# Performance work log

Measured on AMD Instinct MI355X. Metric: run time of the kernel, lower is better.

Reference implementation:

```python
import jax, jax.numpy as jnp
import numpy as np

LN_EPS = 1e-5


def setup_inputs() -> dict:
    key = jax.random.key(0)
    ks = jax.random.split(key, 6)
    N, E, D = 100000, 600000, 128
    x = jax.random.normal(ks[0], (N, D), dtype=jnp.float32)
    edge_index = jax.random.randint(ks[1], (2, E), 0, N, dtype=jnp.int64)
    dropout_mask = jax.random.uniform(ks[2], (N, D), dtype=jnp.float32)
    ln_gamma = jnp.ones((D,), dtype=jnp.float32)
    ln_beta = jnp.zeros((D,), dtype=jnp.float32)
    W_l = jax.random.normal(ks[3], (D, D), dtype=jnp.float32) / np.sqrt(D)
    b_l = jnp.zeros((D,), dtype=jnp.float32)
    W_r = jax.random.normal(ks[4], (D, D), dtype=jnp.float32) / np.sqrt(D)
    return {"x": x, "edge_index": edge_index, "dropout_mask": dropout_mask,
            "ln_gamma": ln_gamma, "ln_beta": ln_beta,
            "W_l": W_l, "b_l": b_l, "W_r": W_r}


def reference(x, edge_index, dropout_mask, ln_gamma, ln_beta, W_l, b_l, W_r):
    N = x.shape[0]
    # LayerNorm (elementwise affine) -> ReLU -> dropout mask
    mu = jnp.mean(x, axis=-1, keepdims=True)
    var = jnp.mean(jnp.square(x - mu), axis=-1, keepdims=True)
    h = (x - mu) * jax.lax.rsqrt(var + LN_EPS) * ln_gamma + ln_beta
    h = jax.nn.relu(h) * dropout_mask  # [N, D]
    # SAGEConv with mean aggregation: messages flow src -> dst
    src, dst = edge_index[0], edge_index[1]
    agg = jax.ops.segment_sum(h[src], dst, num_segments=N)  # [N, D]
    cnt = jax.ops.segment_sum(jnp.ones_like(dst, dtype=h.dtype), dst,
                              num_segments=N)
    mean_agg = agg / jnp.maximum(cnt, 1.0)[:, None]
    # out = lin_l(mean_agg) + lin_r(h); PyG stores weights as [out, in]
    return mean_agg @ W_l.T + b_l + h @ W_r.T
```

## Files before the change

### kernel.cpp

```cpp
#include <hip/hip_runtime.h>

#define LN_EPS 1e-5f
#define D 128
#define SCAN_CHUNK 1024
#define LDSA_STRIDE 264

typedef __attribute__((ext_vector_type(4))) float f32x4;
typedef __attribute__((ext_vector_type(8))) short bf16x8;

static __device__ __forceinline__ ushort f2bf(float f) {
    union { float f; unsigned u; } a; a.f = f;
    unsigned r = a.u + 0x7FFF + ((a.u >> 16) & 1);
    return (ushort)(r >> 16);
}
static __device__ __forceinline__ float bf2f(ushort u) {
    union { unsigned u; float f; } a; a.u = ((unsigned)u) << 16;
    return a.f;
}

__global__ void prep_w(const float* __restrict__ Wl,
                       const float* __restrict__ Wr,
                       ushort* __restrict__ Bfrag) {
    int t = blockIdx.x * blockDim.x + threadIdx.x;
    if (t >= 8 * 8 * 64 * 8) return;
    int i    = t & 7;
    int lane = (t >> 3) & 63;
    int jb   = (t >> 9) & 7;
    int ks   = t >> 12;
    int k = ks * 32 + (lane >> 4) * 8 + i;
    int j = jb * 16 + (lane & 15);
    float v = (k < D) ? Wl[j * D + k] : Wr[j * D + (k - D)];
    Bfrag[t] = f2bf(v);
}

__global__ void ln_hist(const float* __restrict__ x,
                        const float* __restrict__ mask,
                        const float* __restrict__ gamma,
                        const float* __restrict__ beta,
                        ushort* __restrict__ hbf,
                        const int* __restrict__ ei,
                        int* __restrict__ hist,
                        int N, int E, int lnBlocks) {
    if (blockIdx.x >= (unsigned)lnBlocks) {
        int e = (blockIdx.x - lnBlocks) * blockDim.x + threadIdx.x;
        if (e < E) atomicAdd(&hist[ei[E + e]], 1);
        return;
    }
    int node = (blockIdx.x * blockDim.x + threadIdx.x) >> 6;
    int lane = threadIdx.x & 63;
    if (node >= N) return;
    float2 v = ((const float2*)(x + (size_t)node * D))[lane];
    float s  = v.x + v.y;
    float ss = v.x * v.x + v.y * v.y;
#pragma unroll
    for (int off = 32; off > 0; off >>= 1) {
        s  += __shfl_xor(s, off);
        ss += __shfl_xor(ss, off);
    }
    float mu  = s * (1.0f / D);
    float var = ss * (1.0f / D) - mu * mu;
    float rs  = rsqrtf(var + LN_EPS);
    float2 g = ((const float2*)gamma)[lane];
    float2 b = ((const float2*)beta)[lane];
    float2 m = ((const float2*)(mask + (size_t)node * D))[lane];
    ushort2 o;
    o.x = f2bf(fmaxf((v.x - mu) * rs * g.x + b.x, 0.0f) * m.x);
    o.y = f2bf(fmaxf((v.y - mu) * rs * g.y + b.y, 0.0f) * m.y);
    ((ushort2*)(hbf + (size_t)node * D))[lane] = o;
}

__global__ void scan1(const int* __restrict__ hist, int* __restrict__ offs,
                      int* __restrict__ chunk_sums, int N) {
    __shared__ int lds[256];
    int base = blockIdx.x * SCAN_CHUNK;
    int t = threadIdx.x;
    int idx0 = base + t * 4;
    int v[4];
#pragma unroll
    for (int i = 0; i < 4; i++) {
        int idx = idx0 + i;
        v[i] = (idx < N) ? hist[idx] : 0;
    }
    lds[t] = v[0] + v[1] + v[2] + v[3];
    __syncthreads();
    for (int off = 1; off < 256; off <<= 1) {
        int add = (t >= off) ? lds[t - off] : 0;
        __syncthreads();
        lds[t] += add;
        __syncthreads();
    }
    int run = (t == 0) ? 0 : lds[t - 1];
    if (t == 255) chunk_sums[blockIdx.x] = lds[255];
#pragma unroll
    for (int i = 0; i < 4; i++) {
        int idx = idx0 + i;
        if (idx < N) offs[idx] = run;
        run += v[i];
    }
}

__global__ void scan_fix(int* __restrict__ offs, const int* __restrict__ csums,
                         int* __restrict__ cursor, int N) {
    __shared__ int base_s;
    int chunk = (blockIdx.x * 256) / SCAN_CHUNK;
    int t = threadIdx.x;
    if (t < 64) {
        int v = 0;
        for (int c = t; c < chunk; c += 64) v += csums[c];
#pragma unroll
        for (int off = 32; off > 0; off >>= 1) v += __shfl_xor(v, off);
        if (t == 0) base_s = v;
    }
    __syncthreads();
    int i = blockIdx.x * 256 + t;
    if (i >= N) return;
    int v = offs[i] + base_s;
    offs[i] = v;
    cursor[i] = v;
}

__global__ void sort_edges(const int* __restrict__ ei, int* __restrict__ cursor,
                           int* __restrict__ sorted_src, int E) {
    int e = blockIdx.x * blockDim.x + threadIdx.x;
    if (e >= E) return;
    int dst = ei[E + e];
    int pos = atomicAdd(&cursor[dst], 1);
    sorted_src[pos] = ei[e];
}

__global__ void aggregate4(const ushort* __restrict__ hbf,
                           const int* __restrict__ sorted_src,
                           const int* __restrict__ offs,
                           const int* __restrict__ hist,
                           ushort* __restrict__ magg, int N) {
    int wid  = (blockIdx.x * blockDim.x + threadIdx.x) >> 6;
    int lane = threadIdx.x & 63;
    int g  = lane >> 4;
    int sl = lane & 15;
    int node = wid * 4 + g;
    bool valid = node < N;
    int start = 0, deg = 0;
    if (valid) { start = offs[node]; deg = hist[node]; }
    float acc[8];
#pragma unroll
    for (int j = 0; j < 8; j++) acc[j] = 0.0f;
    int i = 0;
    for (; i + 2 <= deg; i += 2) {
        int s0 = sorted_src[start + i];
        int s1 = sorted_src[start + i + 1];
        bf16x8 v0 = *(const bf16x8*)(hbf + (size_t)s0 * D + sl * 8);
        bf16x8 v1 = *(const bf16x8*)(hbf + (size_t)s1 * D + sl * 8);
#pragma unroll
        for (int j = 0; j < 8; j++)
            acc[j] += bf2f((ushort)v0[j]) + bf2f((ushort)v1[j]);
    }
    if (i < deg) {
        int s0 = sorted_src[start + i];
        bf16x8 v0 = *(const bf16x8*)(hbf + (size_t)s0 * D + sl * 8);
#pragma unroll
        for (int j = 0; j < 8; j++) acc[j] += bf2f((ushort)v0[j]);
    }
    if (valid) {
        float inv = 1.0f / fmaxf((float)deg, 1.0f);
        bf16x8 o;
#pragma unroll
        for (int j = 0; j < 8; j++) o[j] = (short)f2bf(acc[j] * inv);
        *(bf16x8*)(magg + (size_t)node * D + sl * 8) = o;
    }
}

__global__ void __launch_bounds__(256, 3)
out_gemm_mfma(float* __restrict__ out,
              const ushort* __restrict__ magg,
              const ushort* __restrict__ hbf,
              const ushort* __restrict__ Bfrag,
              const float* __restrict__ bl,
              int N) {
    __shared__ ushort Alds[64 * LDSA_STRIDE];
    int tid  = threadIdx.x;
    int wave = tid >> 6;
    int lane = tid & 63;
    int n0 = blockIdx.x * 64;

    bf16x8 breg[8][2];
#pragma unroll
    for (int ks = 0; ks < 8; ks++)
#pragma unroll
        for (int jj = 0; jj < 2; jj++) {
            int jb = wave * 2 + jj;
            breg[ks][jj] = *(const bf16x8*)(Bfrag + (size_t)((ks * 8 + jb) * 64 + lane) * 8);
        }

#pragma unroll
    for (int it = 0; it < 4; it++) {
        int chunk = tid + 256 * it;
        int row = chunk >> 4;
        int c8  = chunk & 15;
        int node = n0 + row;
        bf16x8 va = (bf16x8){0,0,0,0,0,0,0,0};
        bf16x8 vh = (bf16x8){0,0,0,0,0,0,0,0};
        if (node < N) {
            va = *(const bf16x8*)(magg + (size_t)node * D + c8 * 8);
            vh = *(const bf16x8*)(hbf  + (size_t)node * D + c8 * 8);
        }
        *(bf16x8*)&Alds[row * LDSA_STRIDE + c8 * 8]       = va;
        *(bf16x8*)&Alds[row * LDSA_STRIDE + 128 + c8 * 8] = vh;
    }
    __syncthreads();

    f32x4 acc[4][2];
#pragma unroll
    for (int nb = 0; nb < 4; nb++)
#pragma unroll
        for (int jj = 0; jj < 2; jj++)
            acc[nb][jj] = (f32x4){0.f, 0.f, 0.f, 0.f};

    int arow = lane & 15;
    int akoff = (lane >> 4) * 8;
#pragma unroll
    for (int ks = 0; ks < 8; ks++) {
#pragma unroll
        for (int nb = 0; nb < 4; nb++) {
            bf16x8 a = *(const bf16x8*)&Alds[(nb * 16 + arow) * LDSA_STRIDE + ks * 32 + akoff];
            acc[nb][0] = __builtin_amdgcn_mfma_f32_16x16x32_bf16(a, breg[ks][0], acc[nb][0], 0, 0, 0);
            acc[nb][1] = __builtin_amdgcn_mfma_f32_16x16x32_bf16(a, breg[ks][1], acc[nb][1], 0, 0, 0);
        }
    }

    float bias0 = bl[wave * 32 + (lane & 15)];
    float bias1 = bl[wave * 32 + 16 + (lane & 15)];
    int rbase = (lane >> 4) * 4;
#pragma unroll
    for (int nb = 0; nb < 4; nb++) {
#pragma unroll
        for (int r = 0; r < 4; r++) {
            int row = nb * 16 + rbase + r;
            if (n0 + row < N) {
                float* orow = out + (size_t)(n0 + row) * D + wave * 32 + (lane & 15);
                orow[0]  = acc[nb][0][r] + bias0;
                orow[16] = acc[nb][1][r] + bias1;
            }
        }
    }
}

extern "C" void kernel_launch(void* const* d_in, const int* in_sizes, int n_in,
                              void* d_out, int out_size, void* d_ws, size_t ws_size,
                              hipStream_t stream) {
    const float* x     = (const float*)d_in[0];
    const int*   ei    = (const int*)  d_in[1];
    const float* mask  = (const float*)d_in[2];
    const float* gamma = (const float*)d_in[3];
    const float* beta  = (const float*)d_in[4];
    const float* Wl    = (const float*)d_in[5];
    const float* bl    = (const float*)d_in[6];
    const float* Wr    = (const float*)d_in[7];
    float* out = (float*)d_out;

    int N = in_sizes[0] / D;
    int E = in_sizes[1] / 2;
    int chunks = (N + SCAN_CHUNK - 1) / SCAN_CHUNK;

    ushort* hbf   = (ushort*)d_ws;
    ushort* magg  = hbf + (size_t)N * D;
    ushort* Bfrag = magg + (size_t)N * D;
    int* hist   = (int*)(Bfrag + 32768);
    int* offs   = hist + N;
    int* cursor = offs + N;
    int* csums  = cursor + N;
    int* ssrc   = csums + 128;

    int lnBlocks = (N + 3) / 4;
    int histBlocks = (E + 255) / 256;

    hipMemsetAsync(hist, 0, (size_t)N * sizeof(int), stream);
    prep_w<<<128, 256, 0, stream>>>(Wl, Wr, Bfrag);
    ln_hist<<<lnBlocks + histBlocks, 256, 0, stream>>>(x, mask, gamma, beta, hbf,
                                                       ei, hist, N, E, lnBlocks);
    scan1<<<chunks, 256, 0, stream>>>(hist, offs, csums, N);
    scan_fix<<<(N + 255) / 256, 256, 0, stream>>>(offs, csums, cursor, N);
    sort_edges<<<(E + 255) / 256, 256, 0, stream>>>(ei, cursor, ssrc, E);
    aggregate4<<<((N + 3) / 4 + 3) / 4, 256, 0, stream>>>(hbf, ssrc, offs, hist, magg, N);
    out_gemm_mfma<<<(N + 63) / 64, 256, 0, stream>>>(out, magg, hbf, Bfrag, bl, N);
}
```

Before: 265.0 us.

## Fuse scan and edge sort into one cooperative kernel, fold memset into prep

Merges the chunk scan, scan fix-up and edge counting-sort into a single cooperative kernel that uses grid-wide syncs, folds the histogram zeroing into the weight-prep kernel, and widens the LayerNorm kernel to float4 with 32 lanes per node. The aim is to cut kernel launches and memset overhead between the small graph-preprocessing stages. In exchange, the sort phase runs on only 256 blocks in a grid-stride loop, and the grid syncs add their own cost.

```diff
diff --git a/kernel.cpp b/kernel.cpp
--- a/kernel.cpp
+++ b/kernel.cpp
@@ -1,4 +1,7 @@
 #include <hip/hip_runtime.h>
+#include <hip/hip_cooperative_groups.h>
+
+namespace cg = cooperative_groups;
 
 #define LN_EPS 1e-5f
 #define D 128
@@ -20,17 +23,23 @@
 
 __global__ void prep_w(const float* __restrict__ Wl,
                        const float* __restrict__ Wr,
-                       ushort* __restrict__ Bfrag) {
-    int t = blockIdx.x * blockDim.x + threadIdx.x;
-    if (t >= 8 * 8 * 64 * 8) return;
-    int i    = t & 7;
-    int lane = (t >> 3) & 63;
-    int jb   = (t >> 9) & 7;
-    int ks   = t >> 12;
-    int k = ks * 32 + (lane >> 4) * 8 + i;
-    int j = jb * 16 + (lane & 15);
-    float v = (k < D) ? Wl[j * D + k] : Wr[j * D + (k - D)];
-    Bfrag[t] = f2bf(v);
+                       ushort* __restrict__ Bfrag,
+                       int* __restrict__ hist, int N) {
+    int idx = blockIdx.x * blockDim.x + threadIdx.x;
+    if (blockIdx.x < 128) {
+        int t = idx;
+        int i    = t & 7;
+        int lane = (t >> 3) & 63;
+        int jb   = (t >> 9) & 7;
+        int ks   = t >> 12;
+        int k = ks * 32 + (lane >> 4) * 8 + i;
+        int j = jb * 16 + (lane & 15);
+        float v = (k < D) ? Wl[j * D + k] : Wr[j * D + (k - D)];
+        Bfrag[t] = f2bf(v);
+    } else {
+        int i = idx - 128 * 256;
+        if (i < N) hist[i] = 0;
+    }
 }
 
 __global__ void ln_hist(const float* __restrict__ x,
@@ -46,86 +55,100 @@
         if (e < E) atomicAdd(&hist[ei[E + e]], 1);
         return;
     }
-    int node = (blockIdx.x * blockDim.x + threadIdx.x) >> 6;
-    int lane = threadIdx.x & 63;
+    int idx  = blockIdx.x * blockDim.x + threadIdx.x;
+    int node = idx >> 5;
+    int sl   = threadIdx.x & 31;
     if (node >= N) return;
-    float2 v = ((const float2*)(x + (size_t)node * D))[lane];
-    float s  = v.x + v.y;
-    float ss = v.x * v.x + v.y * v.y;
-#pragma unroll
-    for (int off = 32; off > 0; off >>= 1) {
+    float4 v = ((const float4*)(x + (size_t)node * D))[sl];
+    float s  = v.x + v.y + v.z + v.w;
+    float ss = fmaf(v.x, v.x, fmaf(v.y, v.y, fmaf(v.z, v.z, v.w * v.w)));
+#pragma unroll
+    for (int off = 16; off > 0; off >>= 1) {
         s  += __shfl_xor(s, off);
         ss += __shfl_xor(ss, off);
     }
     float mu  = s * (1.0f / D);
     float var = ss * (1.0f / D) - mu * mu;
     float rs  = rsqrtf(var + LN_EPS);
-    float2 g = ((const float2*)gamma)[lane];
-    float2 b = ((const float2*)beta)[lane];
-    float2 m = ((const float2*)(mask + (size_t)node * D))[lane];
-    ushort2 o;
+    float4 g = ((const float4*)gamma)[sl];
+    float4 b = ((const float4*)beta)[sl];
+    float4 m = ((const float4*)(mask + (size_t)node * D))[sl];
+    ushort4 o;
     o.x = f2bf(fmaxf((v.x - mu) * rs * g.x + b.x, 0.0f) * m.x);
     o.y = f2bf(fmaxf((v.y - mu) * rs * g.y + b.y, 0.0f) * m.y);
-    ((ushort2*)(hbf + (size_t)node * D))[lane] = o;
-}
-
-__global__ void scan1(const int* __restrict__ hist, int* __restrict__ offs,
-                      int* __restrict__ chunk_sums, int N) {
+    o.z = f2bf(fmaxf((v.z - mu) * rs * g.z + b.z, 0.0f) * m.z);
+    o.w = f2bf(fmaxf((v.w - mu) * rs * g.w + b.w, 0.0f) * m.w);
+    ((ushort4*)(hbf + (size_t)node * D))[sl] = o;
+}
+
+__global__ void scan_sort(const int* __restrict__ ei,
+                          const int* __restrict__ hist,
+                          int* __restrict__ offs,
+                          int* __restrict__ cursor,
+                          int* __restrict__ csums,
+                          int* __restrict__ ssrc,
+                          int N, int E, int chunks) {
+    cg::grid_group grid = cg::this_grid();
     __shared__ int lds[256];
-    int base = blockIdx.x * SCAN_CHUNK;
+    __shared__ int pref[128];
     int t = threadIdx.x;
-    int idx0 = base + t * 4;
-    int v[4];
-#pragma unroll
-    for (int i = 0; i < 4; i++) {
-        int idx = idx0 + i;
-        v[i] = (idx < N) ? hist[idx] : 0;
-    }
-    lds[t] = v[0] + v[1] + v[2] + v[3];
+
+    if (blockIdx.x < (unsigned)chunks) {
+        int base = blockIdx.x * SCAN_CHUNK;
+        int idx0 = base + t * 4;
+        int v[4];
+#pragma unroll
+        for (int i = 0; i < 4; i++) {
+            int idx = idx0 + i;
+            v[i] = (idx < N) ? hist[idx] : 0;
+        }
+        lds[t] = v[0] + v[1] + v[2] + v[3];
+        __syncthreads();
+        for (int off = 1; off < 256; off <<= 1) {
+            int add = (t >= off) ? lds[t - off] : 0;
+            __syncthreads();
+            lds[t] += add;
+            __syncthreads();
+        }
+        int run = (t == 0) ? 0 : lds[t - 1];
+        if (t == 255) csums[blockIdx.x] = lds[255];
+#pragma unroll
+        for (int i = 0; i < 4; i++) {
+            int idx = idx0 + i;
+            if (idx < N) offs[idx] = run;
+            run += v[i];
+        }
+    }
+    __threadfence();
+    grid.sync();
+
+    if (t < 128) pref[t] = (t < chunks) ? csums[t] : 0;
     __syncthreads();
-    for (int off = 1; off < 256; off <<= 1) {
-        int add = (t >= off) ? lds[t - off] : 0;
+    for (int off = 1; off < 128; off <<= 1) {
+        int add = (t < 128 && t >= off) ? pref[t - off] : 0;
         __syncthreads();
-        lds[t] += add;
+        if (t < 128) pref[t] += add;
         __syncthreads();
     }
-    int run = (t == 0) ? 0 : lds[t - 1];
-    if (t == 255) chunk_sums[blockIdx.x] = lds[255];
-#pragma unroll
-    for (int i = 0; i < 4; i++) {
-        int idx = idx0 + i;
-        if (idx < N) offs[idx] = run;
-        run += v[i];
-    }
-}
-
-__global__ void scan_fix(int* __restrict__ offs, const int* __restrict__ csums,
-                         int* __restrict__ cursor, int N) {
-    __shared__ int base_s;
-    int chunk = (blockIdx.x * 256) / SCAN_CHUNK;
-    int t = threadIdx.x;
-    if (t < 64) {
-        int v = 0;
-        for (int c = t; c < chunk; c += 64) v += csums[c];
-#pragma unroll
-        for (int off = 32; off > 0; off >>= 1) v += __shfl_xor(v, off);
-        if (t == 0) base_s = v;
-    }
-    __syncthreads();
-    int i = blockIdx.x * 256 + t;
-    if (i >= N) return;
-    int v = offs[i] + base_s;
-    offs[i] = v;
-    cursor[i] = v;
-}
-
-__global__ void sort_edges(const int* __restrict__ ei, int* __restrict__ cursor,
-                           int* __restrict__ sorted_src, int E) {
-    int e = blockIdx.x * blockDim.x + threadIdx.x;
-    if (e >= E) return;
-    int dst = ei[E + e];
-    int pos = atomicAdd(&cursor[dst], 1);
-    sorted_src[pos] = ei[e];
+    for (int i0 = blockIdx.x * 256; i0 < N; i0 += gridDim.x * 256) {
+        int i = i0 + t;
+        if (i < N) {
+            int c = i >> 10;
+            int b = c ? pref[c - 1] : 0;
+            int v = offs[i] + b;
+            offs[i] = v;
+            cursor[i] = v;
+        }
+    }
+    __threadfence();
+    grid.sync();
+
+    int nth = gridDim.x * blockDim.x;
+    for (int e = blockIdx.x * blockDim.x + t; e < E; e += nth) {
+        int dst = ei[E + e];
+        int pos = atomicAdd(&cursor[dst], 1);
+        ssrc[pos] = ei[e];
+    }
 }
 
 __global__ void aggregate4(const ushort* __restrict__ hbf,
@@ -270,16 +293,19 @@
     int* csums  = cursor + N;
     int* ssrc   = csums + 128;
 
-    int lnBlocks = (N + 3) / 4;
+    int lnBlocks   = (N + 7) / 8;
     int histBlocks = (E + 255) / 256;
 
-    hipMemsetAsync(hist, 0, (size_t)N * sizeof(int), stream);
-    prep_w<<<128, 256, 0, stream>>>(Wl, Wr, Bfrag);
+    prep_w<<<128 + (N + 255) / 256, 256, 0, stream>>>(Wl, Wr, Bfrag, hist, N);
     ln_hist<<<lnBlocks + histBlocks, 256, 0, stream>>>(x, mask, gamma, beta, hbf,
                                                        ei, hist, N, E, lnBlocks);
-    scan1<<<chunks, 256, 0, stream>>>(hist, offs, csums, N);
-    scan_fix<<<(N + 255) / 256, 256, 0, stream>>>(offs, csums, cursor, N);
-    sort_edges<<<(E + 255) / 256, 256, 0, stream>>>(ei, cursor, ssrc, E);
+    {
+        void* args[] = {(void*)&ei, (void*)&hist, (void*)&offs, (void*)&cursor,
+                        (void*)&csums, (void*)&ssrc, (void*)&N, (void*)&E,
+                        (void*)&chunks};
+        hipLaunchCooperativeKernel((void*)scan_sort, dim3(256), dim3(256),
+                                   args, 0, stream);
+    }
     aggregate4<<<((N + 3) / 4 + 3) / 4, 256, 0, stream>>>(hbf, ssrc, offs, hist, magg, N);
     out_gemm_mfma<<<(N + 63) / 64, 256, 0, stream>>>(out, magg, hbf, Bfrag, bl, N);
 }
```

Result: slower. 395.2 us (+49.1%).
